# Kernel optimization log

Measured on AMD Instinct MI355X. Metric: run time of the kernel, lower is better.

## Reference

```python
import jax, jax.numpy as jnp
import numpy as np

N_ATOMS = 1048576
N_CRYS = 8192
NFEA = 128
NCLS = 5
LN_EPS = 1e-5


def setup_inputs() -> dict:
    key = jax.random.key(0)
    k1, k2, k3 = jax.random.split(key, 3)
    data_crys_fea = jax.random.normal(k1, (N_ATOMS, NFEA), dtype=jnp.float32)
    # Contiguous non-empty [start, end) ranges partitioning [0, N_ATOMS)
    rng = np.random.default_rng(0)
    cuts = np.sort(rng.choice(np.arange(1, N_ATOMS), size=N_CRYS - 1, replace=False))
    starts = np.concatenate([[0], cuts])
    ends = np.concatenate([cuts, [N_ATOMS]])
    data_crys_idx = jnp.asarray(np.stack([starts, ends], axis=1).astype(np.int32))
    ln_weight = jnp.ones((NFEA,), dtype=jnp.float32)
    ln_bias = jnp.zeros((NFEA,), dtype=jnp.float32)
    out_w = jax.random.normal(k2, (NCLS, NFEA), dtype=jnp.float32) / np.sqrt(NFEA).astype(np.float32)
    out_b = jax.random.normal(k3, (NCLS,), dtype=jnp.float32) * 0.01
    return {
        "data_crys_fea": data_crys_fea,
        "data_crys_idx": data_crys_idx,
        "ln_weight": ln_weight,
        "ln_bias": ln_bias,
        "out_w": out_w,
        "out_b": out_b,
    }


def reference(data_crys_fea, data_crys_idx, ln_weight, ln_bias, out_w, out_b):
    # --- pool: per-crystal mean over contiguous [start, end) atom ranges ---
    starts = data_crys_idx[:, 0]
    ends = data_crys_idx[:, 1]
    n_atoms = data_crys_fea.shape[0]
    # segment id of each atom via searchsorted on sorted starts
    seg = jnp.searchsorted(starts, jnp.arange(n_atoms, dtype=starts.dtype), side="right") - 1
    seg_sum = jax.ops.segment_sum(data_crys_fea, seg, num_segments=N_CRYS)  # [n_crys, F]
    lens = (ends - starts).astype(data_crys_fea.dtype)
    pooled = seg_sum / lens[:, None]
    # --- LayerNorm over features (biased variance, eps=1e-5, like torch) ---
    mu = jnp.mean(pooled, axis=-1, keepdims=True)
    var = jnp.var(pooled, axis=-1, keepdims=True)
    normed = (pooled - mu) / jnp.sqrt(var + LN_EPS) * ln_weight + ln_bias
    # --- Softplus then Linear ---
    act = jax.nn.softplus(normed)  # [n_crys, F]
    my_output = act @ out_w.T + out_b  # [n_crys, n_cls]
    return my_output, act
```

## Files before the change

kernel.cpp:

```cpp
#include <hip/hip_runtime.h>
#include <hip/hip_bf16.h>

#define NFEA 128
#define NCLS 5
#define LN_EPS 1e-5f
#define CHUNK 128

__global__ __launch_bounds__(256) void seg_partial_kernel(
    const float* __restrict__ fea,
    const int2*  __restrict__ idx,
    float* __restrict__ seg_sum,
    int n_crys)
{
    const int a0 = blockIdx.x * CHUNK;
    const int a1 = a0 + CHUNK;

    int lo = 0, hi = n_crys - 1;
    while (lo < hi) {
        int mid = (lo + hi + 1) >> 1;
        if (idx[mid].x <= a0) lo = mid; else hi = mid - 1;
    }
    int s = lo;

    const int tid = threadIdx.x;
    const int fc  = tid & 31;
    const int al  = tid >> 5;

    const float4* __restrict__ fea4 = (const float4*)fea;
    __shared__ float4 red4[8][32];

    int rs = a0;
    while (rs < a1) {
        const int re = min(idx[s].y, a1);

        float4 acc0 = make_float4(0.f, 0.f, 0.f, 0.f);
        float4 acc1 = make_float4(0.f, 0.f, 0.f, 0.f);
        int a = rs + al;
        for (; a + 8 < re; a += 16) {
            float4 v0 = fea4[(size_t)a * 32 + fc];
            float4 v1 = fea4[(size_t)(a + 8) * 32 + fc];
            acc0.x += v0.x; acc0.y += v0.y; acc0.z += v0.z; acc0.w += v0.w;
            acc1.x += v1.x; acc1.y += v1.y; acc1.z += v1.z; acc1.w += v1.w;
        }
        if (a < re) {
            float4 v = fea4[(size_t)a * 32 + fc];
            acc0.x += v.x; acc0.y += v.y; acc0.z += v.z; acc0.w += v.w;
        }
        acc0.x += acc1.x; acc0.y += acc1.y; acc0.z += acc1.z; acc0.w += acc1.w;

        red4[al][fc] = acc0;
        __syncthreads();
        if (tid < NFEA) {
            const float* redf = (const float*)red4;
            float ssum = 0.f;
            #pragma unroll
            for (int g = 0; g < 8; ++g) ssum += redf[g * NFEA + tid];
            atomicAdd(&seg_sum[(size_t)s * NFEA + tid], ssum);
        }
        __syncthreads();
        rs = re; ++s;
    }
}

__global__ __launch_bounds__(64) void finalize_kernel(
    const float* __restrict__ seg_sum,
    const int2*  __restrict__ idx,
    const float* __restrict__ lnw,
    const float* __restrict__ lnb,
    const float* __restrict__ outw,
    const float* __restrict__ outb,
    float* __restrict__ out_cls,
    float* __restrict__ out_act)
{
    const int c   = blockIdx.x;
    const int tid = threadIdx.x;
    const int2 se = idx[c];
    const float inv_len = 1.f / (float)(se.y - se.x);

    float p0 = seg_sum[(size_t)c * NFEA + tid]      * inv_len;
    float p1 = seg_sum[(size_t)c * NFEA + tid + 64] * inv_len;

    float t = p0 + p1;
    #pragma unroll
    for (int off = 32; off; off >>= 1) t += __shfl_xor(t, off);
    const float mu = t * (1.f / NFEA);

    const float d0 = p0 - mu, d1 = p1 - mu;
    float v = d0 * d0 + d1 * d1;
    #pragma unroll
    for (int off = 32; off; off >>= 1) v += __shfl_xor(v, off);
    const float rstd = rsqrtf(v * (1.f / NFEA) + LN_EPS);

    const float x0 = d0 * rstd * lnw[tid]      + lnb[tid];
    const float x1 = d1 * rstd * lnw[tid + 64] + lnb[tid + 64];
    const float a0 = (x0 > 0.f) ? x0 + log1pf(expf(-x0)) : log1pf(expf(x0));
    const float a1 = (x1 > 0.f) ? x1 + log1pf(expf(-x1)) : log1pf(expf(x1));

    out_act[(size_t)c * NFEA + tid]      = a0;
    out_act[(size_t)c * NFEA + tid + 64] = a1;

    #pragma unroll
    for (int k = 0; k < NCLS; ++k) {
        float p = a0 * outw[k * NFEA + tid] + a1 * outw[k * NFEA + tid + 64];
        #pragma unroll
        for (int off = 32; off; off >>= 1) p += __shfl_xor(p, off);
        if (tid == k) out_cls[(size_t)c * NCLS + k] = p + outb[k];
    }
}

extern "C" void kernel_launch(void* const* d_in, const int* in_sizes, int n_in,
                              void* d_out, int out_size, void* d_ws, size_t ws_size,
                              hipStream_t stream) {
    const float* fea  = (const float*)d_in[0];
    const int2*  idx  = (const int2*)d_in[1];
    const float* lnw  = (const float*)d_in[2];
    const float* lnb  = (const float*)d_in[3];
    const float* outw = (const float*)d_in[4];
    const float* outb = (const float*)d_in[5];

    const int n_crys  = in_sizes[1] / 2;
    const int n_atoms = in_sizes[0] / NFEA;

    float* seg_sum = (float*)d_ws;
    float* out_cls = (float*)d_out;
    float* out_act = (float*)d_out + (size_t)n_crys * NCLS;

    hipMemsetAsync(seg_sum, 0, (size_t)n_crys * NFEA * sizeof(float), stream);

    seg_partial_kernel<<<n_atoms / CHUNK, 256, 0, stream>>>(fea, idx, seg_sum, n_crys);
    finalize_kernel<<<n_crys, 64, 0, stream>>>(seg_sum, idx, lnw, lnb, outw, outb,
                                               out_cls, out_act);
}
```

Baseline: 123.9 us.

## Use per-wave atom slabs with precomputed segment map and shuffle reduction

Replaces the per-block binary search with a prep kernel that zeroes the accumulator and builds a slab-to-segment lookup table. It also assigns 64-atom slabs to individual wavefronts, so the shared-memory reduction and __syncthreads become a cross-half shuffle. The inner loop is software-pipelined with four accumulators, and finalize packs four crystals per 256-thread block. The cost is more atomics, since each wave issues its own per-segment atomicAdds, plus an extra kernel launch.

```diff
diff --git a/kernel.cpp b/kernel.cpp
--- a/kernel.cpp
+++ b/kernel.cpp
@@ -4,65 +4,103 @@
 #define NFEA 128
 #define NCLS 5
 #define LN_EPS 1e-5f
-#define CHUNK 128
+#define WCHUNK 64
+
+__global__ __launch_bounds__(256) void prep_kernel(
+    const int2* __restrict__ idx,
+    int*  __restrict__ seg_of_slab,
+    float* __restrict__ seg_sum,
+    int n_crys)
+{
+    const int t    = blockIdx.x * 256 + threadIdx.x;
+    const int nthr = gridDim.x * 256;
+
+    float4* z = (float4*)seg_sum;
+    const int nz = n_crys * NFEA / 4;
+    for (int i = t; i < nz; i += nthr) z[i] = make_float4(0.f, 0.f, 0.f, 0.f);
+
+    if (t < n_crys) {
+        const int2 se = idx[t];
+        int j = (se.x + WCHUNK - 1) / WCHUNK;
+        for (; j * WCHUNK < se.y; ++j) seg_of_slab[j] = t;
+    }
+}
 
 __global__ __launch_bounds__(256) void seg_partial_kernel(
     const float* __restrict__ fea,
     const int2*  __restrict__ idx,
-    float* __restrict__ seg_sum,
-    int n_crys)
+    const int*   __restrict__ seg_of_slab,
+    float* __restrict__ seg_sum)
 {
-    const int a0 = blockIdx.x * CHUNK;
-    const int a1 = a0 + CHUNK;
+    const int gw   = (blockIdx.x * 256 + threadIdx.x) >> 6;
+    const int lane = threadIdx.x & 63;
+    const int fc   = lane & 31;
+    const int al   = lane >> 5;
+    const int a0   = gw * WCHUNK;
+    const int a1   = a0 + WCHUNK;
 
-    int lo = 0, hi = n_crys - 1;
-    while (lo < hi) {
-        int mid = (lo + hi + 1) >> 1;
-        if (idx[mid].x <= a0) lo = mid; else hi = mid - 1;
-    }
-    int s = lo;
-
-    const int tid = threadIdx.x;
-    const int fc  = tid & 31;
-    const int al  = tid >> 5;
-
+    int s = seg_of_slab[gw];
     const float4* __restrict__ fea4 = (const float4*)fea;
-    __shared__ float4 red4[8][32];
 
     int rs = a0;
     while (rs < a1) {
         const int re = min(idx[s].y, a1);
 
-        float4 acc0 = make_float4(0.f, 0.f, 0.f, 0.f);
-        float4 acc1 = make_float4(0.f, 0.f, 0.f, 0.f);
+        float4 acc0 = make_float4(0.f,0.f,0.f,0.f);
+        float4 acc1 = make_float4(0.f,0.f,0.f,0.f);
+        float4 acc2 = make_float4(0.f,0.f,0.f,0.f);
+        float4 acc3 = make_float4(0.f,0.f,0.f,0.f);
+
         int a = rs + al;
-        for (; a + 8 < re; a += 16) {
-            float4 v0 = fea4[(size_t)a * 32 + fc];
-            float4 v1 = fea4[(size_t)(a + 8) * 32 + fc];
+        if (a + 6 < re) {
+            float4 v0 = fea4[(size_t)a       * 32 + fc];
+            float4 v1 = fea4[(size_t)(a + 2) * 32 + fc];
+            float4 v2 = fea4[(size_t)(a + 4) * 32 + fc];
+            float4 v3 = fea4[(size_t)(a + 6) * 32 + fc];
+            a += 8;
+            for (; a + 6 < re; a += 8) {
+                float4 n0 = fea4[(size_t)a       * 32 + fc];
+                float4 n1 = fea4[(size_t)(a + 2) * 32 + fc];
+                float4 n2 = fea4[(size_t)(a + 4) * 32 + fc];
+                float4 n3 = fea4[(size_t)(a + 6) * 32 + fc];
+                acc0.x += v0.x; acc0.y += v0.y; acc0.z += v0.z; acc0.w += v0.w;
+                acc1.x += v1.x; acc1.y += v1.y; acc1.z += v1.z; acc1.w += v1.w;
+                acc2.x += v2.x; acc2.y += v2.y; acc2.z += v2.z; acc2.w += v2.w;
+                acc3.x += v3.x; acc3.y += v3.y; acc3.z += v3.z; acc3.w += v3.w;
+                v0 = n0; v1 = n1; v2 = n2; v3 = n3;
+            }
             acc0.x += v0.x; acc0.y += v0.y; acc0.z += v0.z; acc0.w += v0.w;
             acc1.x += v1.x; acc1.y += v1.y; acc1.z += v1.z; acc1.w += v1.w;
+            acc2.x += v2.x; acc2.y += v2.y; acc2.z += v2.z; acc2.w += v2.w;
+            acc3.x += v3.x; acc3.y += v3.y; acc3.z += v3.z; acc3.w += v3.w;
         }
-        if (a < re) {
+        for (; a < re; a += 2) {
             float4 v = fea4[(size_t)a * 32 + fc];
             acc0.x += v.x; acc0.y += v.y; acc0.z += v.z; acc0.w += v.w;
         }
-        acc0.x += acc1.x; acc0.y += acc1.y; acc0.z += acc1.z; acc0.w += acc1.w;
 
-        red4[al][fc] = acc0;
-        __syncthreads();
-        if (tid < NFEA) {
-            const float* redf = (const float*)red4;
-            float ssum = 0.f;
-            #pragma unroll
-            for (int g = 0; g < 8; ++g) ssum += redf[g * NFEA + tid];
-            atomicAdd(&seg_sum[(size_t)s * NFEA + tid], ssum);
+        acc0.x += acc1.x + acc2.x + acc3.x;
+        acc0.y += acc1.y + acc2.y + acc3.y;
+        acc0.z += acc1.z + acc2.z + acc3.z;
+        acc0.w += acc1.w + acc2.w + acc3.w;
+
+        acc0.x += __shfl_xor(acc0.x, 32);
+        acc0.y += __shfl_xor(acc0.y, 32);
+        acc0.z += __shfl_xor(acc0.z, 32);
+        acc0.w += __shfl_xor(acc0.w, 32);
+
+        if (lane < 32) {
+            float* dst = &seg_sum[(size_t)s * NFEA + lane * 4];
+            atomicAdd(dst + 0, acc0.x);
+            atomicAdd(dst + 1, acc0.y);
+            atomicAdd(dst + 2, acc0.z);
+            atomicAdd(dst + 3, acc0.w);
         }
-        __syncthreads();
         rs = re; ++s;
     }
 }
 
-__global__ __launch_bounds__(64) void finalize_kernel(
+__global__ __launch_bounds__(256) void finalize_kernel(
     const float* __restrict__ seg_sum,
     const int2*  __restrict__ idx,
     const float* __restrict__ lnw,
@@ -72,8 +110,8 @@
     float* __restrict__ out_cls,
     float* __restrict__ out_act)
 {
-    const int c   = blockIdx.x;
-    const int tid = threadIdx.x;
+    const int c   = (blockIdx.x * 256 + threadIdx.x) >> 6;
+    const int tid = threadIdx.x & 63;
     const int2 se = idx[c];
     const float inv_len = 1.f / (float)(se.y - se.x);
 
@@ -120,14 +158,16 @@
 
     const int n_crys  = in_sizes[1] / 2;
     const int n_atoms = in_sizes[0] / NFEA;
+    const int nslab   = n_atoms / WCHUNK;
 
-    float* seg_sum = (float*)d_ws;
+    float* seg_sum     = (float*)d_ws;
+    int*   seg_of_slab = (int*)((char*)d_ws + (size_t)n_crys * NFEA * sizeof(float));
+
     float* out_cls = (float*)d_out;
     float* out_act = (float*)d_out + (size_t)n_crys * NCLS;
 
-    hipMemsetAsync(seg_sum, 0, (size_t)n_crys * NFEA * sizeof(float), stream);
-
-    seg_partial_kernel<<<n_atoms / CHUNK, 256, 0, stream>>>(fea, idx, seg_sum, n_crys);
-    finalize_kernel<<<n_crys, 64, 0, stream>>>(seg_sum, idx, lnw, lnb, outw, outb,
-                                               out_cls, out_act);
+    prep_kernel<<<128, 256, 0, stream>>>(idx, seg_of_slab, seg_sum, n_crys);
+    seg_partial_kernel<<<nslab / 4, 256, 0, stream>>>(fea, idx, seg_of_slab, seg_sum);
+    finalize_kernel<<<n_crys / 4, 256, 0, stream>>>(seg_sum, idx, lnw, lnb, outw, outb,
+                                                    out_cls, out_act);
 }
```

Measured after the change: 129.7 us. +4.7%, slower.

## Fuse finalize into pooling for chunk-interior crystals, handle straddlers separately

Applied to the files above, without the earlier changes.

Grows the atom chunk per block from 128 to 1024. Crystals that lie wholly inside one chunk are now pooled, layer-normed, softplus-activated and projected inside the pooling kernel, with no atomics or global round trip. Only crystals that cross a chunk boundary still use atomics and are finished by a separate straddler kernel. The inner loop is also software-pipelined four loads deep. The cost is fewer blocks (1024) and a serial finalize step inside each block, which may lower parallelism and the load traffic in flight on a large GPU.

```diff
diff --git a/kernel.cpp b/kernel.cpp
--- a/kernel.cpp
+++ b/kernel.cpp
@@ -4,82 +4,14 @@
 #define NFEA 128
 #define NCLS 5
 #define LN_EPS 1e-5f
-#define CHUNK 128
+#define CHUNK 1024
 
-__global__ __launch_bounds__(256) void seg_partial_kernel(
-    const float* __restrict__ fea,
-    const int2*  __restrict__ idx,
-    float* __restrict__ seg_sum,
-    int n_crys)
+__device__ __forceinline__ void finalize_crystal(
+    int lane, int c, float p0, float p1,
+    const float* __restrict__ lnw, const float* __restrict__ lnb,
+    const float* __restrict__ outw, const float* __restrict__ outb,
+    float* __restrict__ out_cls, float* __restrict__ out_act)
 {
-    const int a0 = blockIdx.x * CHUNK;
-    const int a1 = a0 + CHUNK;
-
-    int lo = 0, hi = n_crys - 1;
-    while (lo < hi) {
-        int mid = (lo + hi + 1) >> 1;
-        if (idx[mid].x <= a0) lo = mid; else hi = mid - 1;
-    }
-    int s = lo;
-
-    const int tid = threadIdx.x;
-    const int fc  = tid & 31;
-    const int al  = tid >> 5;
-
-    const float4* __restrict__ fea4 = (const float4*)fea;
-    __shared__ float4 red4[8][32];
-
-    int rs = a0;
-    while (rs < a1) {
-        const int re = min(idx[s].y, a1);
-
-        float4 acc0 = make_float4(0.f, 0.f, 0.f, 0.f);
-        float4 acc1 = make_float4(0.f, 0.f, 0.f, 0.f);
-        int a = rs + al;
-        for (; a + 8 < re; a += 16) {
-            float4 v0 = fea4[(size_t)a * 32 + fc];
-            float4 v1 = fea4[(size_t)(a + 8) * 32 + fc];
-            acc0.x += v0.x; acc0.y += v0.y; acc0.z += v0.z; acc0.w += v0.w;
-            acc1.x += v1.x; acc1.y += v1.y; acc1.z += v1.z; acc1.w += v1.w;
-        }
-        if (a < re) {
-            float4 v = fea4[(size_t)a * 32 + fc];
-            acc0.x += v.x; acc0.y += v.y; acc0.z += v.z; acc0.w += v.w;
-        }
-        acc0.x += acc1.x; acc0.y += acc1.y; acc0.z += acc1.z; acc0.w += acc1.w;
-
-        red4[al][fc] = acc0;
-        __syncthreads();
-        if (tid < NFEA) {
-            const float* redf = (const float*)red4;
-            float ssum = 0.f;
-            #pragma unroll
-            for (int g = 0; g < 8; ++g) ssum += redf[g * NFEA + tid];
-            atomicAdd(&seg_sum[(size_t)s * NFEA + tid], ssum);
-        }
-        __syncthreads();
-        rs = re; ++s;
-    }
-}
-
-__global__ __launch_bounds__(64) void finalize_kernel(
-    const float* __restrict__ seg_sum,
-    const int2*  __restrict__ idx,
-    const float* __restrict__ lnw,
-    const float* __restrict__ lnb,
-    const float* __restrict__ outw,
-    const float* __restrict__ outb,
-    float* __restrict__ out_cls,
-    float* __restrict__ out_act)
-{
-    const int c   = blockIdx.x;
-    const int tid = threadIdx.x;
-    const int2 se = idx[c];
-    const float inv_len = 1.f / (float)(se.y - se.x);
-
-    float p0 = seg_sum[(size_t)c * NFEA + tid]      * inv_len;
-    float p1 = seg_sum[(size_t)c * NFEA + tid + 64] * inv_len;
-
     float t = p0 + p1;
     #pragma unroll
     for (int off = 32; off; off >>= 1) t += __shfl_xor(t, off);
@@ -91,21 +23,132 @@
     for (int off = 32; off; off >>= 1) v += __shfl_xor(v, off);
     const float rstd = rsqrtf(v * (1.f / NFEA) + LN_EPS);
 
-    const float x0 = d0 * rstd * lnw[tid]      + lnb[tid];
-    const float x1 = d1 * rstd * lnw[tid + 64] + lnb[tid + 64];
+    const float x0 = d0 * rstd * lnw[lane]      + lnb[lane];
+    const float x1 = d1 * rstd * lnw[lane + 64] + lnb[lane + 64];
     const float a0 = (x0 > 0.f) ? x0 + log1pf(expf(-x0)) : log1pf(expf(x0));
     const float a1 = (x1 > 0.f) ? x1 + log1pf(expf(-x1)) : log1pf(expf(x1));
 
-    out_act[(size_t)c * NFEA + tid]      = a0;
-    out_act[(size_t)c * NFEA + tid + 64] = a1;
+    out_act[(size_t)c * NFEA + lane]      = a0;
+    out_act[(size_t)c * NFEA + lane + 64] = a1;
 
     #pragma unroll
     for (int k = 0; k < NCLS; ++k) {
-        float p = a0 * outw[k * NFEA + tid] + a1 * outw[k * NFEA + tid + 64];
+        float p = a0 * outw[k * NFEA + lane] + a1 * outw[k * NFEA + lane + 64];
         #pragma unroll
         for (int off = 32; off; off >>= 1) p += __shfl_xor(p, off);
-        if (tid == k) out_cls[(size_t)c * NCLS + k] = p + outb[k];
+        if (lane == k) out_cls[(size_t)c * NCLS + k] = p + outb[k];
     }
+}
+
+__global__ __launch_bounds__(256) void fused_pool_kernel(
+    const float* __restrict__ fea,
+    const int2*  __restrict__ idx,
+    float* __restrict__ seg_sum,
+    const float* __restrict__ lnw, const float* __restrict__ lnb,
+    const float* __restrict__ outw, const float* __restrict__ outb,
+    float* __restrict__ out_cls, float* __restrict__ out_act,
+    int n_crys)
+{
+    const int c0 = blockIdx.x * CHUNK;
+    const int c1 = c0 + CHUNK;
+    const int tid = threadIdx.x;
+    const int fc  = tid & 31;
+    const int al  = tid >> 5;
+
+    int lo = 0, hi = n_crys - 1;
+    while (lo < hi) {
+        int mid = (lo + hi + 1) >> 1;
+        if (idx[mid].x <= c0) lo = mid; else hi = mid - 1;
+    }
+    int s = lo;
+
+    const float4* __restrict__ fea4 = (const float4*)fea;
+    __shared__ float4 red4[8][32];
+    __shared__ float pooledA[NFEA];
+
+    int rs = c0;
+    while (rs < c1) {
+        const int2 se = idx[s];
+        const int re = min(se.y, c1);
+
+        float4 acc0 = make_float4(0.f,0.f,0.f,0.f);
+        float4 acc1 = make_float4(0.f,0.f,0.f,0.f);
+        float4 acc2 = make_float4(0.f,0.f,0.f,0.f);
+        float4 acc3 = make_float4(0.f,0.f,0.f,0.f);
+
+        int a = rs + al;
+        if (a + 24 < re) {
+            float4 v0 = fea4[(size_t)a        * 32 + fc];
+            float4 v1 = fea4[(size_t)(a + 8)  * 32 + fc];
+            float4 v2 = fea4[(size_t)(a + 16) * 32 + fc];
+            float4 v3 = fea4[(size_t)(a + 24) * 32 + fc];
+            a += 32;
+            for (; a + 24 < re; a += 32) {
+                float4 n0 = fea4[(size_t)a        * 32 + fc];
+                float4 n1 = fea4[(size_t)(a + 8)  * 32 + fc];
+                float4 n2 = fea4[(size_t)(a + 16) * 32 + fc];
+                float4 n3 = fea4[(size_t)(a + 24) * 32 + fc];
+                acc0.x += v0.x; acc0.y += v0.y; acc0.z += v0.z; acc0.w += v0.w;
+                acc1.x += v1.x; acc1.y += v1.y; acc1.z += v1.z; acc1.w += v1.w;
+                acc2.x += v2.x; acc2.y += v2.y; acc2.z += v2.z; acc2.w += v2.w;
+                acc3.x += v3.x; acc3.y += v3.y; acc3.z += v3.z; acc3.w += v3.w;
+                v0 = n0; v1 = n1; v2 = n2; v3 = n3;
+            }
+            acc0.x += v0.x; acc0.y += v0.y; acc0.z += v0.z; acc0.w += v0.w;
+            acc1.x += v1.x; acc1.y += v1.y; acc1.z += v1.z; acc1.w += v1.w;
+            acc2.x += v2.x; acc2.y += v2.y; acc2.z += v2.z; acc2.w += v2.w;
+            acc3.x += v3.x; acc3.y += v3.y; acc3.z += v3.z; acc3.w += v3.w;
+        }
+        for (; a < re; a += 8) {
+            float4 v = fea4[(size_t)a * 32 + fc];
+            acc0.x += v.x; acc0.y += v.y; acc0.z += v.z; acc0.w += v.w;
+        }
+        acc0.x += acc1.x + acc2.x + acc3.x;
+        acc0.y += acc1.y + acc2.y + acc3.y;
+        acc0.z += acc1.z + acc2.z + acc3.z;
+        acc0.w += acc1.w + acc2.w + acc3.w;
+
+        red4[al][fc] = acc0;
+        __syncthreads();
+
+        const bool interior = (se.x >= c0) && (se.y <= c1);
+        if (tid < NFEA) {
+            const float* redf = (const float*)red4;
+            float ssum = 0.f;
+            #pragma unroll
+            for (int g = 0; g < 8; ++g) ssum += redf[g * NFEA + tid];
+            if (interior) pooledA[tid] = ssum;
+            else          atomicAdd(&seg_sum[(size_t)s * NFEA + tid], ssum);
+        }
+        __syncthreads();
+
+        if (interior && tid < 64) {
+            const float inv_len = 1.f / (float)(se.y - se.x);
+            finalize_crystal(tid, s, pooledA[tid] * inv_len, pooledA[tid + 64] * inv_len,
+                             lnw, lnb, outw, outb, out_cls, out_act);
+        }
+        rs = re; ++s;
+    }
+}
+
+__global__ __launch_bounds__(256) void straddler_kernel(
+    const float* __restrict__ seg_sum,
+    const int2*  __restrict__ idx,
+    const float* __restrict__ lnw, const float* __restrict__ lnb,
+    const float* __restrict__ outw, const float* __restrict__ outb,
+    float* __restrict__ out_cls, float* __restrict__ out_act,
+    int n_crys)
+{
+    const int c    = (blockIdx.x * 256 + threadIdx.x) >> 6;
+    const int lane = threadIdx.x & 63;
+    if (c >= n_crys) return;
+    const int2 se = idx[c];
+    if ((se.x / CHUNK) == ((se.y - 1) / CHUNK)) return;
+
+    const float inv_len = 1.f / (float)(se.y - se.x);
+    const float p0 = seg_sum[(size_t)c * NFEA + lane]      * inv_len;
+    const float p1 = seg_sum[(size_t)c * NFEA + lane + 64] * inv_len;
+    finalize_crystal(lane, c, p0, p1, lnw, lnb, outw, outb, out_cls, out_act);
 }
 
 extern "C" void kernel_launch(void* const* d_in, const int* in_sizes, int n_in,
@@ -127,7 +170,9 @@
 
     hipMemsetAsync(seg_sum, 0, (size_t)n_crys * NFEA * sizeof(float), stream);
 
-    seg_partial_kernel<<<n_atoms / CHUNK, 256, 0, stream>>>(fea, idx, seg_sum, n_crys);
-    finalize_kernel<<<n_crys, 64, 0, stream>>>(seg_sum, idx, lnw, lnb, outw, outb,
-                                               out_cls, out_act);
+    fused_pool_kernel<<<n_atoms / CHUNK, 256, 0, stream>>>(
+        fea, idx, seg_sum, lnw, lnb, outw, outb, out_cls, out_act, n_crys);
+
+    straddler_kernel<<<(n_crys * 64 + 255) / 256, 256, 0, stream>>>(
+        seg_sum, idx, lnw, lnb, outw, outb, out_cls, out_act, n_crys);
 }
```

New measurement: 155.3 us. +25.3%, slower.
